# Optimization experiments

Measured on AMD Instinct MI355X. Metric: run time of the kernel, lower is better.

The kernel has to match this reference:

```python
import jax, jax.numpy as jnp
import numpy as np

B, C, H, W = 8, 512, 48, 48
DK = C // 8            # query/key dim
L = max(H, W)          # rel_pos_length == H == W
R = 2 * L - 1          # num relative shifts
N = H * W
EPS = 1e-5


def setup_inputs() -> dict:
    key = jax.random.key(0)
    ks = jax.random.split(key, 20)
    d = {
        "x": jax.random.normal(ks[0], (B, C, H, W), jnp.float32),
        "Wq": jax.random.normal(ks[1], (DK, C), jnp.float32) * 0.02,
        "bq": jnp.zeros((DK,), jnp.float32),
        "q_scale": jnp.ones((DK,), jnp.float32),
        "q_bias": jnp.zeros((DK,), jnp.float32),
        "Wk": jax.random.normal(ks[2], (DK, C), jnp.float32) * 0.02,
        "bk": jnp.zeros((DK,), jnp.float32),
        "k_scale": jnp.ones((DK,), jnp.float32),
        "k_bias": jnp.zeros((DK,), jnp.float32),
        "Wv": jax.random.normal(ks[3], (C, C), jnp.float32) * 0.02,
        "bv": jnp.zeros((C,), jnp.float32),
        "v_scale": jnp.ones((C,), jnp.float32),
        "v_bias": jnp.zeros((C,), jnp.float32),
        "rel_rows": jax.random.normal(ks[4], (R, DK), jnp.float32),
        "rel_columns": jax.random.normal(ks[5], (R, DK), jnp.float32),
        "bnr_scale": jnp.ones((C,), jnp.float32),
        "bnr_bias": jnp.zeros((C,), jnp.float32),
        "bnc_scale": jnp.ones((C,), jnp.float32),
        "bnc_bias": jnp.zeros((C,), jnp.float32),
        # gamma is a learned scalar (init 0 in torch; nonzero here so output != x)
        "gamma": jax.random.normal(ks[6], (1,), jnp.float32) * 0.1,
    }
    return d


def _bn(y, scale, bias):
    # train-mode BatchNorm2d: batch stats over (B,H,W), biased variance
    m = jnp.mean(y, axis=(0, 2, 3))
    v = jnp.mean((y - m[None, :, None, None]) ** 2, axis=(0, 2, 3))
    yn = (y - m[None, :, None, None]) * jax.lax.rsqrt(v + EPS)[None, :, None, None]
    return yn * scale[None, :, None, None] + bias[None, :, None, None]


def _conv_bn_relu(x, Wc, bc, scale, bias):
    y = jnp.einsum('bchw,oc->bohw', x, Wc) + bc[None, :, None, None]  # 1x1 conv
    return jax.nn.relu(_bn(y, scale, bias))


def _rel_P(l, rel_table):
    # compute_reindexing_tensor reduces to a one-hot over shift (i - x) since
    # |i-x| <= L always holds when L == l; Ih @ rel_table == gather by shift.
    x = jnp.arange(l)[:, None]
    i = jnp.arange(l)[None, :]
    idx = i - x + (L - 1)                 # (l, l) in [0, 2L-2]
    return rel_table[idx]                 # (l, l, DK)


def reference(x, Wq, bq, q_scale, q_bias, Wk, bk, k_scale, k_bias,
              Wv, bv, v_scale, v_bias, rel_rows, rel_columns,
              bnr_scale, bnr_bias, bnc_scale, bnc_bias, gamma):
    q = _conv_bn_relu(x, Wq, bq, q_scale, q_bias).reshape(B, DK, N)   # proj_query^T
    k = _conv_bn_relu(x, Wk, bk, k_scale, k_bias).reshape(B, DK, N)
    v = _conv_bn_relu(x, Wv, bv, v_scale, v_bias).reshape(B, C, N)

    energy = jnp.einsum('bdn,bdm->bnm', q, k)        # (B,N,N) = Q^T K (unscaled)
    attention = jax.nn.softmax(energy, axis=-1)
    out = jnp.einsum('bcj,bij->bci', v, attention)   # V A^T
    attn_mask = out.reshape(B, C, H, W)

    # relative position terms: Eh = V (Ph Q^T), Ew = V (Pw Q^T)
    Ph = _rel_P(H, rel_rows).reshape(N, DK)          # (N,DK) since H==W
    Mh = jnp.einsum('nd,bdm->bnm', Ph, q)
    Eh = jnp.einsum('bcn,bnm->bcm', v, Mh).reshape(B, C, H, W)
    Eh = _bn(Eh, bnr_scale, bnr_bias)

    Pw = _rel_P(W, rel_columns).reshape(N, DK)
    Mw = jnp.einsum('nd,bdm->bnm', Pw, q)
    Ew = jnp.einsum('bcn,bnm->bcm', v, Mw).reshape(B, C, H, W)
    Ew = _bn(Ew, bnc_scale, bnc_bias)

    attn_mask = attn_mask + Eh + Ew
    return gamma[0] * attn_mask + x
```

## Files before the change

### kernel.cpp

```cpp
#include <hip/hip_runtime.h>
#include <math.h>

#define BB   8
#define CIN  512
#define NSP  2304
#define OCH  640
#define LL   48

typedef __attribute__((ext_vector_type(8))) short bf16x8;
typedef __attribute__((ext_vector_type(8))) unsigned short u16x8;
typedef __attribute__((ext_vector_type(4))) float f32x4;

__device__ inline unsigned short f2bf(float f) {
  unsigned int u = __float_as_uint(f);
  unsigned int r = (u + 0x7fffu + ((u >> 16) & 1u)) >> 16;
  return (unsigned short)r;
}
__device__ inline float bf2f(unsigned short h) {
  return __uint_as_float(((unsigned int)h) << 16);
}


#define STAGE128x64(GP, LD, LDSN)                                              \
  {                                                                            \
    const unsigned short* gsrc_ = (GP);                                        \
    _Pragma("unroll") for (int cc_ = 0; cc_ < 4; cc_++) {                      \
      int base_ = w * 2048 + cc_ * 512;                                        \
      int row_ = w * 32 + cc_ * 8 + rsub;                                      \
      __builtin_amdgcn_global_load_lds(                                        \
          (const __attribute__((address_space(1))) void*)(gsrc_ +              \
              (size_t)row_ * (LD) + scolb),                                    \
          (__attribute__((address_space(3))) void*)&(LDSN)[base_], 16, 0, 0);  \
    }                                                                          \
  }

#define MFMA_STEP(APTR, BPTR)                                                  \
  _Pragma("unroll") for (int kk_ = 0; kk_ < 2; kk_++) {                        \
    bf16x8 af_[4], bf_[4];                                                     \
    int kcol_ = (((kk_ * 4 + (lane >> 4)) ^ (lane & 7)) * 8);                  \
    _Pragma("unroll") for (int m_ = 0; m_ < 4; m_++)                           \
      af_[m_] = *(const bf16x8*)&(APTR)[(wr * 64 + m_ * 16 + (lane & 15)) * 64 + kcol_]; \
    _Pragma("unroll") for (int n_ = 0; n_ < 4; n_++)                           \
      bf_[n_] = *(const bf16x8*)&(BPTR)[(wc * 64 + n_ * 16 + (lane & 15)) * 64 + kcol_]; \
    _Pragma("unroll") for (int m_ = 0; m_ < 4; m_++)                           \
      _Pragma("unroll") for (int n_ = 0; n_ < 4; n_++)                         \
        acc[m_][n_] = __builtin_amdgcn_mfma_f32_16x16x32_bf16(                 \
            af_[m_], bf_[n_], acc[m_][n_], 0, 0, 0);                           \
  }

#define MFMA_PROLOG()                                                          \
  const int tid = threadIdx.x;                                                 \
  const int lane = tid & 63;                                                   \
  const int w = tid >> 6;                                                      \
  const int wr = w >> 1, wc = w & 1;                                           \
  const int rsub = lane >> 3;                                                  \
  const int scolb = ((lane & 7) ^ rsub) * 8;                                   \
  f32x4 acc[4][4] = {};                                                        \
  (void)scolb; (void)rsub;

__global__ __launch_bounds__(256) void prep_all(
    const float* __restrict__ Wq, const float* __restrict__ bq,
    const float* __restrict__ Wk, const float* __restrict__ bk,
    const float* __restrict__ Wv, const float* __restrict__ bv,
    const float* __restrict__ rel_rows, const float* __restrict__ rel_cols,
    unsigned short* __restrict__ Wstb, float* __restrict__ bst,
    unsigned short* __restrict__ Pcatb) {
  int idx = blockIdx.x * 256 + threadIdx.x;
  if (idx < OCH * CIN) {
    int row = idx >> 9;
    float val;
    if (row < 64)       val = Wq[idx];
    else if (row < 128) val = Wk[idx - (64 << 9)];
    else                val = Wv[idx - (128 << 9)];
    Wstb[idx] = f2bf(val);
    if (idx < OCH) {
      float bval;
      if (idx < 64)       bval = bq[idx];
      else if (idx < 128) bval = bk[idx - 64];
      else                bval = bv[idx - 128];
      bst[idx] = bval;
    }
  } else {
    int p = idx - OCH * CIN;
    int dd = p / NSP;
    int n = p - dd * NSP;
    int xr = n / LL;
    int ic = n - xr * LL;
    int shift = ic - xr + (LL - 1);
    float val = (dd < 64) ? rel_rows[shift * 64 + dd]
                          : rel_cols[shift * 64 + (dd - 64)];
    Pcatb[p] = f2bf(val);
  }
}

__global__ __launch_bounds__(256) void transpose_x(
    const float* __restrict__ x, unsigned short* __restrict__ xTb) {
  __shared__ float t[64][65];
  const int n0 = blockIdx.x * 64;
  const int c0 = blockIdx.y * 64;
  const int b = blockIdx.z;
  const int j = threadIdx.x & 63;
  const int g = threadIdx.x >> 6;
  const float* xp = x + (size_t)b * CIN * NSP;
#pragma unroll
  for (int i = 0; i < 16; i++) {
    int cl = g * 16 + i;
    t[cl][j] = xp[(size_t)(c0 + cl) * NSP + n0 + j];
  }
  __syncthreads();
  unsigned short* op = xTb + (size_t)b * NSP * CIN;
#pragma unroll
  for (int i = 0; i < 16; i++) {
    int nl = g * 16 + i;
    op[(size_t)(n0 + nl) * CIN + c0 + j] = f2bf(t[j][nl]);
  }
}

__global__ __launch_bounds__(256) void proj_mfma(
    const unsigned short* __restrict__ Wstb, const float* __restrict__ bst,
    const unsigned short* __restrict__ xTb, unsigned short* __restrict__ y16,
    float* __restrict__ part1, float* __restrict__ part2) {
  __shared__ unsigned short As[8192];
  __shared__ unsigned short Bs[8192];
  int sw = ((blockIdx.x & 7) * 90) + (blockIdx.x >> 3);
  const int rb = sw % 5;
  const int nb = (sw / 5) % 18;
  const int b = sw / 90;
  const int r0 = rb * 128;
  const int n0 = nb * 128;
  MFMA_PROLOG();
  const unsigned short* A = Wstb + (size_t)r0 * CIN;
  const unsigned short* B = xTb + (size_t)b * NSP * CIN + (size_t)n0 * CIN;
  for (int k0 = 0; k0 < CIN; k0 += 64) {
    STAGE128x64(A + k0, CIN, As);
    STAGE128x64(B + k0, CIN, Bs);
    __syncthreads();
    MFMA_STEP(As, Bs);
    __syncthreads();
  }
  float* sp = (float*)As;
#pragma unroll
  for (int m = 0; m < 4; m++) {
#pragma unroll
    for (int r = 0; r < 4; r++) {
      int rl = wr * 64 + m * 16 + (lane >> 4) * 4 + r;
      int row = r0 + rl;
      float bias = bst[row];
      float s1 = 0.f, s2 = 0.f;
#pragma unroll
      for (int n = 0; n < 4; n++) {
        float yv = acc[m][n][r] + bias;
        s1 += yv;
        s2 += yv * yv;
        y16[((size_t)b * OCH + row) * NSP + n0 + wc * 64 + n * 16 + (lane & 15)] = f2bf(yv);
      }
#pragma unroll
      for (int off = 1; off < 16; off <<= 1) {
        s1 += __shfl_xor(s1, off);
        s2 += __shfl_xor(s2, off);
      }
      if ((lane & 15) == 0) {
        sp[rl * 2 + wc] = s1;
        sp[256 + rl * 2 + wc] = s2;
      }
    }
  }
  __syncthreads();
  if (tid < 128) {
    size_t pbase = ((size_t)b * 18 + nb) * OCH + r0 + tid;
    part1[pbase] = sp[tid * 2] + sp[tid * 2 + 1];
    part2[pbase] = sp[256 + tid * 2] + sp[256 + tid * 2 + 1];
  }
}

__global__ __launch_bounds__(256) void bn_finalize(
    const float* __restrict__ part1, const float* __restrict__ part2,
    const float* __restrict__ qs_, const float* __restrict__ qb_,
    const float* __restrict__ ks_, const float* __restrict__ kb_,
    const float* __restrict__ vs_, const float* __restrict__ vb_,
    float* __restrict__ chanA, float* __restrict__ chanB) {
  const int ch = blockIdx.x;
  const int tid = threadIdx.x;
  float s1 = 0.f, s2 = 0.f;
  for (int t = tid; t < 144; t += 256) {
    s1 += part1[(size_t)t * OCH + ch];
    s2 += part2[(size_t)t * OCH + ch];
  }
  __shared__ float sb[8];
#pragma unroll
  for (int off = 32; off > 0; off >>= 1) {
    s1 += __shfl_down(s1, off);
    s2 += __shfl_down(s2, off);
  }
  int lane = tid & 63, wid = tid >> 6;
  if (lane == 0) { sb[wid] = s1; sb[4 + wid] = s2; }
  __syncthreads();
  if (tid == 0) {
    float ts  = sb[0] + sb[1] + sb[2] + sb[3];
    float ts2 = sb[4] + sb[5] + sb[6] + sb[7];
    const float inv = 1.f / (float)(BB * NSP);
    float mean = ts * inv;
    float var  = ts2 * inv - mean * mean;
    float scale, bias;
    if (ch < 64)       { scale = qs_[ch];       bias = qb_[ch]; }
    else if (ch < 128) { scale = ks_[ch - 64];  bias = kb_[ch - 64]; }
    else               { scale = vs_[ch - 128]; bias = vb_[ch - 128]; }
    float a = scale * rsqrtf(var + 1e-5f);
    chanA[ch] = a;
    chanB[ch] = bias - mean * a;
  }
}

__global__ __launch_bounds__(256) void bnrelu_all(
    unsigned short* __restrict__ y16, const float* __restrict__ chanA,
    const float* __restrict__ chanB) {
  size_t i = ((size_t)blockIdx.x * 256 + threadIdx.x) * 8;
  int ch = (int)((i / NSP) % OCH);
  float a = chanA[ch], bo = chanB[ch];
  ushort4 u0 = *(ushort4*)&y16[i];
  ushort4 u1 = *(ushort4*)&y16[i + 4];
  ushort4 o0, o1;
  o0.x = f2bf(fmaxf(0.f, a * bf2f(u0.x) + bo));
  o0.y = f2bf(fmaxf(0.f, a * bf2f(u0.y) + bo));
  o0.z = f2bf(fmaxf(0.f, a * bf2f(u0.z) + bo));
  o0.w = f2bf(fmaxf(0.f, a * bf2f(u0.w) + bo));
  o1.x = f2bf(fmaxf(0.f, a * bf2f(u1.x) + bo));
  o1.y = f2bf(fmaxf(0.f, a * bf2f(u1.y) + bo));
  o1.z = f2bf(fmaxf(0.f, a * bf2f(u1.z) + bo));
  o1.w = f2bf(fmaxf(0.f, a * bf2f(u1.w) + bo));
  *(ushort4*)&y16[i] = o0;
  *(ushort4*)&y16[i + 4] = o1;
}

__global__ __launch_bounds__(256) void tr_qk(
    const unsigned short* __restrict__ y16, unsigned short* __restrict__ qTb,
    unsigned short* __restrict__ kTb) {
  __shared__ unsigned short t[64][72];
  const int n0 = blockIdx.x * 64;
  const int qk = blockIdx.y;
  const int b = blockIdx.z;
  const int j = threadIdx.x & 63;
  const int g = threadIdx.x >> 6;
#pragma unroll
  for (int i = 0; i < 16; i++) {
    int cl = g * 16 + i;
    t[cl][j] = y16[((size_t)b * OCH + qk * 64 + cl) * NSP + n0 + j];
  }
  __syncthreads();
  unsigned short* out = (qk == 0) ? qTb : kTb;
#pragma unroll
  for (int i = 0; i < 16; i++) {
    int nl = g * 16 + i;
    out[((size_t)b * NSP + n0 + nl) * 64 + j] = t[j][nl];
  }
}

__global__ __launch_bounds__(256) void qsum_kernel(
    const unsigned short* __restrict__ y16, float* __restrict__ qs) {
  int bd = blockIdx.x;
  int b = bd >> 6, d = bd & 63;
  const ushort4* p = (const ushort4*)(y16 + ((size_t)b * OCH + d) * NSP);
  float s = 0.f;
  for (int t = threadIdx.x; t < NSP / 4; t += 256) {
    ushort4 u = p[t];
    s += bf2f(u.x) + bf2f(u.y) + bf2f(u.z) + bf2f(u.w);
  }
  __shared__ float sb[4];
#pragma unroll
  for (int off = 32; off > 0; off >>= 1) s += __shfl_down(s, off);
  int lane = threadIdx.x & 63, wid = threadIdx.x >> 6;
  if (lane == 0) sb[wid] = s;
  __syncthreads();
  if (threadIdx.x == 0) qs[bd] = sb[0] + sb[1] + sb[2] + sb[3];
}

__global__ __launch_bounds__(256) void gq_mfma(
    const unsigned short* __restrict__ y16, float* __restrict__ Gqp) {
  __shared__ float wlds[4 * 4096];
  const int bx = blockIdx.x;
  const int b = bx >> 2, kc = bx & 3;
  const int tid = threadIdx.x;
  const int lane = tid & 63;
  const int w = tid >> 6;
  const unsigned short* q = y16 + (size_t)b * OCH * NSP;
  f32x4 acc[4][4] = {};
  for (int k0 = kc * 576 + w * 32; k0 < (kc + 1) * 576; k0 += 128) {
    bf16x8 fr[4];
#pragma unroll
    for (int f = 0; f < 4; f++) {
      int row = f * 16 + (lane & 15);
      fr[f] = *(const bf16x8*)&q[(size_t)row * NSP + k0 + (lane >> 4) * 8];
    }
#pragma unroll
    for (int fm = 0; fm < 4; fm++)
#pragma unroll
      for (int fn = 0; fn < 4; fn++)
        acc[fm][fn] = __builtin_amdgcn_mfma_f32_16x16x32_bf16(
            fr[fm], fr[fn], acc[fm][fn], 0, 0, 0);
  }
#pragma unroll
  for (int fm = 0; fm < 4; fm++)
#pragma unroll
    for (int fn = 0; fn < 4; fn++)
#pragma unroll
      for (int r = 0; r < 4; r++) {
        int d = fm * 16 + (lane >> 4) * 4 + r;
        int e = fn * 16 + (lane & 15);
        wlds[w * 4096 + d * 64 + e] = acc[fm][fn][r];
      }
  __syncthreads();
  for (int t = tid; t < 4096; t += 256)
    Gqp[(size_t)bx * 4096 + t] =
        wlds[t] + wlds[4096 + t] + wlds[8192 + t] + wlds[12288 + t];
}

__global__ __launch_bounds__(256) void energy_mfma(
    const unsigned short* __restrict__ qTb, const unsigned short* __restrict__ kTb,
    unsigned short* __restrict__ Pp, float* __restrict__ Ppart) {
  __shared__ unsigned short As[8192];
  __shared__ unsigned short Bs[8192];
  int sw = ((blockIdx.x & 7) * 324) + (blockIdx.x >> 3);
  const int jb = sw % 18;
  const int ib = (sw / 18) % 18;
  const int b = sw / 324;
  const int i0 = ib * 128;
  const int j0 = jb * 128;
  MFMA_PROLOG();
  STAGE128x64(qTb + ((size_t)b * NSP + i0) * 64, 64, As);
  STAGE128x64(kTb + ((size_t)b * NSP + j0) * 64, 64, Bs);
  __syncthreads();
  MFMA_STEP(As, Bs);
  __syncthreads();
  float* sp = (float*)As;
  unsigned short* pp = Pp + (size_t)b * NSP * NSP;
#pragma unroll
  for (int m = 0; m < 4; m++) {
#pragma unroll
    for (int r = 0; r < 4; r++) {
      int rl = wr * 64 + m * 16 + (lane >> 4) * 4 + r;
      int i = i0 + rl;
      float s1 = 0.f;
#pragma unroll
      for (int n = 0; n < 4; n++) {
        int j = j0 + wc * 64 + n * 16 + (lane & 15);
        unsigned short h = f2bf(__expf(acc[m][n][r]));
        pp[(size_t)i * NSP + j] = h;
        s1 += bf2f(h);
      }
#pragma unroll
      for (int off = 1; off < 16; off <<= 1) s1 += __shfl_xor(s1, off);
      if ((lane & 15) == 0) sp[rl * 2 + wc] = s1;
    }
  }
  __syncthreads();
  if (tid < 128)
    Ppart[((size_t)b * 18 + jb) * NSP + i0 + tid] = sp[tid * 2] + sp[tid * 2 + 1];
}

__global__ __launch_bounds__(256) void zred_kernel(
    const float* __restrict__ Ppart, float* __restrict__ rZ) {
  int row = blockIdx.x * 256 + threadIdx.x;
  int b = row / NSP, i = row % NSP;
  float s = 0.f;
#pragma unroll
  for (int jb = 0; jb < 18; jb++) s += Ppart[((size_t)b * 18 + jb) * NSP + i];
  rZ[row] = 1.f / s;
}

__global__ __launch_bounds__(256) void up_mfma(
    const unsigned short* __restrict__ y16, const unsigned short* __restrict__ Pcatb,
    float* __restrict__ Upart) {
  __shared__ unsigned short As[8192];
  __shared__ unsigned short Bs[8192];
  int sw = ((blockIdx.x & 7) * 24) + (blockIdx.x >> 3);
  const int cb = sw % 4;
  const int kc = (sw / 4) % 6;
  const int b = sw / 24;
  const int c0 = cb * 128;
  MFMA_PROLOG();
  const unsigned short* A = y16 + ((size_t)b * OCH + 128 + c0) * NSP;
  for (int k0 = kc * 384; k0 < kc * 384 + 384; k0 += 64) {
    STAGE128x64(A + k0, NSP, As);
    STAGE128x64(Pcatb + k0, NSP, Bs);
    __syncthreads();
    MFMA_STEP(As, Bs);
    __syncthreads();
  }
  float* up = Upart + ((size_t)kc * BB + b) * CIN * 128 + (size_t)c0 * 128;
#pragma unroll
  for (int m = 0; m < 4; m++)
#pragma unroll
    for (int r = 0; r < 4; r++) {
      int rl = wr * 64 + m * 16 + (lane >> 4) * 4 + r;
#pragma unroll
      for (int n = 0; n < 4; n++) {
        int col = wc * 64 + n * 16 + (lane & 15);
        up[(size_t)rl * 128 + col] = acc[m][n][r];
      }
    }
}

__global__ __launch_bounds__(256) void up_reduce(
    const float* __restrict__ Upart, float* __restrict__ Ucat) {
  size_t idx = (size_t)blockIdx.x * 256 + threadIdx.x;
  float s = 0.f;
#pragma unroll
  for (int kc = 0; kc < 6; kc++) s += Upart[(size_t)kc * 524288 + idx];
  Ucat[idx] = s;
}

__global__ __launch_bounds__(64) void rel_stats(
    const float* __restrict__ Ucat, const float* __restrict__ Gqp,
    const float* __restrict__ qs,
    const float* __restrict__ bnr_s, const float* __restrict__ bnr_b,
    const float* __restrict__ bnc_s, const float* __restrict__ bnc_b,
    float* __restrict__ gh, float* __restrict__ gw, float* __restrict__ offc) {
  const int c = blockIdx.x;
  const int d = threadIdx.x;
  __shared__ float su[2][64];
  float s1h = 0.f, s2h = 0.f, s1w = 0.f, s2w = 0.f;
  for (int b = 0; b < BB; b++) {
    size_t base = ((size_t)b * CIN + c) * 128;
    float uh = Ucat[base + d];
    float uw = Ucat[base + 64 + d];
    __syncthreads();
    su[0][d] = uh;
    su[1][d] = uw;
    __syncthreads();
    float th = 0.f, tw = 0.f;
#pragma unroll
    for (int kc = 0; kc < 4; kc++) {
      const float* G = Gqp + ((size_t)(b * 4 + kc)) * 4096 + d * 64;
      for (int e = 0; e < 64; e++) {
        float g = G[e];
        th += g * su[0][e];
        tw += g * su[1][e];
      }
    }
    float qsd = qs[b * 64 + d];
    s1h += uh * qsd;
    s2h += uh * th;
    s1w += uw * qsd;
    s2w += uw * tw;
  }
#pragma unroll
  for (int off = 32; off > 0; off >>= 1) {
    s1h += __shfl_down(s1h, off);
    s2h += __shfl_down(s2h, off);
    s1w += __shfl_down(s1w, off);
    s2w += __shfl_down(s2w, off);
  }
  if (d == 0) {
    const float inv = 1.f / (float)(BB * NSP);
    float mh = s1h * inv, vh = s2h * inv - mh * mh;
    float mw = s1w * inv, vw = s2w * inv - mw * mw;
    float gch = bnr_s[c] * rsqrtf(vh + 1e-5f);
    float gcw = bnc_s[c] * rsqrtf(vw + 1e-5f);
    gh[c] = gch;
    gw[c] = gcw;
    offc[c] = (bnr_b[c] - mh * gch) + (bnc_b[c] - mw * gcw);
  }
}

__global__ __launch_bounds__(256) void combine_u(
    const float* __restrict__ Ucat, const float* __restrict__ gh,
    const float* __restrict__ gw, unsigned short* __restrict__ Ucb) {
  int idx = blockIdx.x * 256 + threadIdx.x;
  int d = idx & 63;
  int c = (idx >> 6) & 511;
  int b = idx >> 15;
  size_t base = ((size_t)b * CIN + c) * 128;
  Ucb[idx] = f2bf(Ucat[base + d] * gh[c] + Ucat[base + 64 + d] * gw[c]);
}

__global__ __launch_bounds__(256) void attn_fused_gemm(
    const unsigned short* __restrict__ y16,
    const unsigned short* __restrict__ Pp,
    const float* __restrict__ rZ,
    const unsigned short* __restrict__ Ucb,
    const unsigned short* __restrict__ qTb,
    const float* __restrict__ offc,
    const float* __restrict__ gammap,
    const float* __restrict__ x,
    float* __restrict__ dst) {
  __shared__ unsigned short As[2][8192];
  __shared__ unsigned short Bs[2][8192];
  int sw = ((blockIdx.x & 7) * 72) + (blockIdx.x >> 3);
  const int cb = sw % 4;
  const int ib = (sw / 4) % 18;
  const int b = sw / 72;
  const int c0 = cb * 128;
  const int i0 = ib * 128;
  MFMA_PROLOG();
  const unsigned short* A = y16 + ((size_t)b * OCH + 128 + c0) * NSP;
  const unsigned short* B = Pp + (size_t)b * NSP * NSP + (size_t)i0 * NSP;
  const unsigned short* A2 = Ucb + (size_t)b * CIN * 64 + (size_t)c0 * 64;
  const unsigned short* B2 = qTb + (size_t)b * NSP * 64 + (size_t)i0 * 64;

  STAGE128x64(A, NSP, As[0]);
  STAGE128x64(B, NSP, Bs[0]);
  STAGE128x64(A + 64, NSP, As[1]);
  STAGE128x64(B + 64, NSP, Bs[1]);
  asm volatile("s_waitcnt vmcnt(8)" ::: "memory");
  __builtin_amdgcn_sched_barrier(0);
  __builtin_amdgcn_s_barrier();

  int cur = 0;
  for (int tt = 0; tt < 37; ++tt) {
    if (tt == 36) {
#pragma unroll
      for (int n = 0; n < 4; n++) {
        float rz = rZ[(size_t)b * NSP + i0 + wc * 64 + n * 16 + (lane & 15)];
#pragma unroll
        for (int m = 0; m < 4; m++)
#pragma unroll
          for (int r = 0; r < 4; r++) acc[m][n][r] *= rz;
      }
    }
    __builtin_amdgcn_s_setprio(1);
    MFMA_STEP(As[cur], Bs[cur]);
    __builtin_amdgcn_s_setprio(0);
    __builtin_amdgcn_sched_barrier(0);
    __builtin_amdgcn_s_barrier();
    if (tt + 2 < 36) {
      STAGE128x64(A + (tt + 2) * 64, NSP, As[cur]);
      STAGE128x64(B + (tt + 2) * 64, NSP, Bs[cur]);
      asm volatile("s_waitcnt vmcnt(8)" ::: "memory");
    } else if (tt + 2 == 36) {
      STAGE128x64(A2, 64, As[cur]);
      STAGE128x64(B2, 64, Bs[cur]);
      asm volatile("s_waitcnt vmcnt(8)" ::: "memory");
    } else {
      asm volatile("s_waitcnt vmcnt(0)" ::: "memory");
    }
    __builtin_amdgcn_sched_barrier(0);
    __builtin_amdgcn_s_barrier();
    cur ^= 1;
  }

  const float gmm = gammap[0];
  const float* xp = x + (size_t)b * CIN * NSP;
  float* dp = dst + (size_t)b * CIN * NSP;
#pragma unroll
  for (int m = 0; m < 4; m++) {
#pragma unroll
    for (int r = 0; r < 4; r++) {
      int c = c0 + wr * 64 + m * 16 + (lane >> 4) * 4 + r;
      float off = offc[c];
#pragma unroll
      for (int n = 0; n < 4; n++) {
        int i = i0 + wc * 64 + n * 16 + (lane & 15);
        size_t o = (size_t)c * NSP + i;
        dp[o] = gmm * (acc[m][n][r] + off) + xp[o];
      }
    }
  }
}

extern "C" void kernel_launch(void* const* d_in, const int* in_sizes, int n_in,
                              void* d_out, int out_size, void* d_ws, size_t ws_size,
                              hipStream_t stream) {
  const float* x        = (const float*)d_in[0];
  const float* Wq       = (const float*)d_in[1];
  const float* bq       = (const float*)d_in[2];
  const float* q_scale  = (const float*)d_in[3];
  const float* q_bias   = (const float*)d_in[4];
  const float* Wk       = (const float*)d_in[5];
  const float* bk       = (const float*)d_in[6];
  const float* k_scale  = (const float*)d_in[7];
  const float* k_bias   = (const float*)d_in[8];
  const float* Wv       = (const float*)d_in[9];
  const float* bv       = (const float*)d_in[10];
  const float* v_scale  = (const float*)d_in[11];
  const float* v_bias   = (const float*)d_in[12];
  const float* rel_rows = (const float*)d_in[13];
  const float* rel_cols = (const float*)d_in[14];
  const float* bnr_s    = (const float*)d_in[15];
  const float* bnr_b    = (const float*)d_in[16];
  const float* bnc_s    = (const float*)d_in[17];
  const float* bnc_b    = (const float*)d_in[18];
  const float* gamma    = (const float*)d_in[19];
  float* dst = (float*)d_out;

  float* ws = (float*)d_ws;
  size_t o = 0;
  unsigned short* Wstb = (unsigned short*)(ws + o); o += (size_t)OCH * CIN / 2;
  float* bst    = ws + o; o += 1024;
  float* chanA  = ws + o; o += 1024;
  float* chanB  = ws + o; o += 1024;
  unsigned short* Pcatb = (unsigned short*)(ws + o); o += (size_t)128 * NSP / 2;
  unsigned short* y16 = (unsigned short*)(ws + o); o += (size_t)BB * OCH * NSP / 2;
  unsigned short* xTb = (unsigned short*)(ws + o); o += (size_t)BB * NSP * CIN / 2;
  unsigned short* Pp  = (unsigned short*)(ws + o); o += (size_t)BB * NSP * NSP / 2;
  float* Ppart  = ws + o; o += (size_t)BB * 18 * NSP;
  float* rZ     = ws + o; o += (size_t)BB * NSP;
  float* Upart  = ws + o; o += (size_t)6 * BB * CIN * 128;
  float* Ucat   = ws + o; o += (size_t)BB * CIN * 128;
  float* Gqp    = ws + o; o += (size_t)32 * 4096;
  float* part1  = ws + o; o += (size_t)BB * 18 * OCH;
  float* part2  = ws + o; o += (size_t)BB * 18 * OCH;
  float* qs     = ws + o; o += 1024;
  float* gh     = ws + o; o += 1024;
  float* gw     = ws + o; o += 1024;
  float* offc   = ws + o; o += 1024;
  unsigned short* qTb = (unsigned short*)(ws + o); o += (size_t)BB * NSP * 64 / 2;
  unsigned short* kTb = (unsigned short*)(ws + o); o += (size_t)BB * NSP * 64 / 2;
  unsigned short* Ucb = (unsigned short*)(ws + o); o += (size_t)BB * CIN * 64 / 2;

  prep_all<<<(OCH * CIN + 128 * NSP) / 256, 256, 0, stream>>>(
      Wq, bq, Wk, bk, Wv, bv, rel_rows, rel_cols, Wstb, bst, Pcatb);
  transpose_x<<<dim3(NSP / 64, CIN / 64, BB), 256, 0, stream>>>(x, xTb);

  proj_mfma<<<720, 256, 0, stream>>>(Wstb, bst, xTb, y16, part1, part2);
  bn_finalize<<<OCH, 256, 0, stream>>>(part1, part2, q_scale, q_bias, k_scale,
                                       k_bias, v_scale, v_bias, chanA, chanB);
  bnrelu_all<<<(int)((size_t)BB * OCH * NSP / 8 / 256), 256, 0, stream>>>(y16, chanA, chanB);
  tr_qk<<<dim3(NSP / 64, 2, BB), 256, 0, stream>>>(y16, qTb, kTb);
  qsum_kernel<<<BB * 64, 256, 0, stream>>>(y16, qs);
  gq_mfma<<<32, 256, 0, stream>>>(y16, Gqp);

  energy_mfma<<<2592, 256, 0, stream>>>(qTb, kTb, Pp, Ppart);
  zred_kernel<<<BB * NSP / 256, 256, 0, stream>>>(Ppart, rZ);

  up_mfma<<<192, 256, 0, stream>>>(y16, Pcatb, Upart);
  up_reduce<<<2048, 256, 0, stream>>>(Upart, Ucat);
  rel_stats<<<CIN, 64, 0, stream>>>(Ucat, Gqp, qs, bnr_s, bnr_b, bnc_s, bnc_b,
                                    gh, gw, offc);
  combine_u<<<(BB * CIN * 64) / 256, 256, 0, stream>>>(Ucat, gh, gw, Ucb);

  attn_fused_gemm<<<576, 256, 0, stream>>>(y16, Pp, rZ, Ucb, qTb, offc, gamma, x, dst);
}
```

Measured before the change: 249.8 us.

## Double-buffer proj/up GEMMs, fuse rel-stats kernels, use 512-thread attention blocks

The projection and up GEMMs switch from a load-sync-compute loop with a single LDS buffer to a double-buffered prefetch pipeline with raised wave priority, so global loads overlap with MFMA work. The up_reduce, rel_stats and combine_u kernels are merged into one rel_finalize kernel, which removes two launches and the Ucat round trip through global memory. The final attention GEMM moves to 512 threads per block, with 8 waves each computing a 64x32 sub-tile and half the waves staging A while the other half stage B. The trade is more LDS per block and fewer accumulators per wave, which changes how many blocks fit per CU and how much latency each wave can hide.

```diff
diff --git a/kernel.cpp b/kernel.cpp
--- a/kernel.cpp
+++ b/kernel.cpp
@@ -31,6 +31,32 @@
           (const __attribute__((address_space(1))) void*)(gsrc_ +              \
               (size_t)row_ * (LD) + scolb),                                    \
           (__attribute__((address_space(3))) void*)&(LDSN)[base_], 16, 0, 0);  \
+    }                                                                          \
+  }
+
+#define STAGE8(GPA, LDA, LA, GPB, LDB, LB)                                     \
+  {                                                                            \
+    if (w < 4) {                                                               \
+      const unsigned short* gsrc_ = (GPA);                                     \
+      _Pragma("unroll") for (int cc_ = 0; cc_ < 4; cc_++) {                    \
+        int base_ = w * 2048 + cc_ * 512;                                      \
+        int row_ = w * 32 + cc_ * 8 + rsub;                                    \
+        __builtin_amdgcn_global_load_lds(                                      \
+            (const __attribute__((address_space(1))) void*)(gsrc_ +            \
+                (size_t)row_ * (LDA) + scolb),                                 \
+            (__attribute__((address_space(3))) void*)&(LA)[base_], 16, 0, 0);  \
+      }                                                                        \
+    } else {                                                                   \
+      const unsigned short* gsrc_ = (GPB);                                     \
+      int w2_ = w - 4;                                                         \
+      _Pragma("unroll") for (int cc_ = 0; cc_ < 4; cc_++) {                    \
+        int base_ = w2_ * 2048 + cc_ * 512;                                    \
+        int row_ = w2_ * 32 + cc_ * 8 + rsub;                                  \
+        __builtin_amdgcn_global_load_lds(                                      \
+            (const __attribute__((address_space(1))) void*)(gsrc_ +            \
+                (size_t)row_ * (LDB) + scolb),                                 \
+            (__attribute__((address_space(3))) void*)&(LB)[base_], 16, 0, 0);  \
+      }                                                                        \
     }                                                                          \
   }
 
@@ -48,6 +74,20 @@
             af_[m_], bf_[n_], acc[m_][n_], 0, 0, 0);                           \
   }
 
+#define MFMA_STEP8(APTR, BPTR)                                                 \
+  _Pragma("unroll") for (int kk_ = 0; kk_ < 2; kk_++) {                        \
+    bf16x8 af_[4], bf_[2];                                                     \
+    int kcol_ = (((kk_ * 4 + (lane >> 4)) ^ (lane & 7)) * 8);                  \
+    _Pragma("unroll") for (int m_ = 0; m_ < 4; m_++)                           \
+      af_[m_] = *(const bf16x8*)&(APTR)[(wr * 64 + m_ * 16 + (lane & 15)) * 64 + kcol_]; \
+    _Pragma("unroll") for (int n_ = 0; n_ < 2; n_++)                           \
+      bf_[n_] = *(const bf16x8*)&(BPTR)[(wc * 32 + n_ * 16 + (lane & 15)) * 64 + kcol_]; \
+    _Pragma("unroll") for (int m_ = 0; m_ < 4; m_++)                           \
+      _Pragma("unroll") for (int n_ = 0; n_ < 2; n_++)                         \
+        acc[m_][n_] = __builtin_amdgcn_mfma_f32_16x16x32_bf16(                 \
+            af_[m_], bf_[n_], acc[m_][n_], 0, 0, 0);                           \
+  }
+
 #define MFMA_PROLOG()                                                          \
   const int tid = threadIdx.x;                                                 \
   const int lane = tid & 63;                                                   \
@@ -56,7 +96,7 @@
   const int rsub = lane >> 3;                                                  \
   const int scolb = ((lane & 7) ^ rsub) * 8;                                   \
   f32x4 acc[4][4] = {};                                                        \
-  (void)scolb; (void)rsub;
+  (void)scolb; (void)rsub; (void)wr; (void)wc;
 
 __global__ __launch_bounds__(256) void prep_all(
     const float* __restrict__ Wq, const float* __restrict__ bq,
@@ -120,8 +160,8 @@
     const unsigned short* __restrict__ Wstb, const float* __restrict__ bst,
     const unsigned short* __restrict__ xTb, unsigned short* __restrict__ y16,
     float* __restrict__ part1, float* __restrict__ part2) {
-  __shared__ unsigned short As[8192];
-  __shared__ unsigned short Bs[8192];
+  __shared__ unsigned short As[2][8192];
+  __shared__ unsigned short Bs[2][8192];
   int sw = ((blockIdx.x & 7) * 90) + (blockIdx.x >> 3);
   const int rb = sw % 5;
   const int nb = (sw / 5) % 18;
@@ -131,14 +171,35 @@
   MFMA_PROLOG();
   const unsigned short* A = Wstb + (size_t)r0 * CIN;
   const unsigned short* B = xTb + (size_t)b * NSP * CIN + (size_t)n0 * CIN;
-  for (int k0 = 0; k0 < CIN; k0 += 64) {
-    STAGE128x64(A + k0, CIN, As);
-    STAGE128x64(B + k0, CIN, Bs);
-    __syncthreads();
-    MFMA_STEP(As, Bs);
-    __syncthreads();
-  }
-  float* sp = (float*)As;
+
+  STAGE128x64(A, CIN, As[0]);
+  STAGE128x64(B, CIN, Bs[0]);
+  STAGE128x64(A + 64, CIN, As[1]);
+  STAGE128x64(B + 64, CIN, Bs[1]);
+  asm volatile("s_waitcnt vmcnt(8)" ::: "memory");
+  __builtin_amdgcn_sched_barrier(0);
+  __builtin_amdgcn_s_barrier();
+
+  int cur = 0;
+  for (int t = 0; t < 8; ++t) {
+    __builtin_amdgcn_s_setprio(1);
+    MFMA_STEP(As[cur], Bs[cur]);
+    __builtin_amdgcn_s_setprio(0);
+    __builtin_amdgcn_sched_barrier(0);
+    __builtin_amdgcn_s_barrier();
+    if (t + 2 < 8) {
+      STAGE128x64(A + (t + 2) * 64, CIN, As[cur]);
+      STAGE128x64(B + (t + 2) * 64, CIN, Bs[cur]);
+      asm volatile("s_waitcnt vmcnt(8)" ::: "memory");
+    } else {
+      asm volatile("s_waitcnt vmcnt(0)" ::: "memory");
+    }
+    __builtin_amdgcn_sched_barrier(0);
+    __builtin_amdgcn_s_barrier();
+    cur ^= 1;
+  }
+
+  float* sp = (float*)&As[0][0];
 #pragma unroll
   for (int m = 0; m < 4; m++) {
 #pragma unroll
@@ -370,22 +431,44 @@
 __global__ __launch_bounds__(256) void up_mfma(
     const unsigned short* __restrict__ y16, const unsigned short* __restrict__ Pcatb,
     float* __restrict__ Upart) {
-  __shared__ unsigned short As[8192];
-  __shared__ unsigned short Bs[8192];
+  __shared__ unsigned short As[2][8192];
+  __shared__ unsigned short Bs[2][8192];
   int sw = ((blockIdx.x & 7) * 24) + (blockIdx.x >> 3);
   const int cb = sw % 4;
   const int kc = (sw / 4) % 6;
   const int b = sw / 24;
   const int c0 = cb * 128;
   MFMA_PROLOG();
-  const unsigned short* A = y16 + ((size_t)b * OCH + 128 + c0) * NSP;
-  for (int k0 = kc * 384; k0 < kc * 384 + 384; k0 += 64) {
-    STAGE128x64(A + k0, NSP, As);
-    STAGE128x64(Pcatb + k0, NSP, Bs);
-    __syncthreads();
-    MFMA_STEP(As, Bs);
-    __syncthreads();
-  }
+  const unsigned short* A = y16 + ((size_t)b * OCH + 128 + c0) * NSP + kc * 384;
+  const unsigned short* B = Pcatb + kc * 384;
+
+  STAGE128x64(A, NSP, As[0]);
+  STAGE128x64(B, NSP, Bs[0]);
+  STAGE128x64(A + 64, NSP, As[1]);
+  STAGE128x64(B + 64, NSP, Bs[1]);
+  asm volatile("s_waitcnt vmcnt(8)" ::: "memory");
+  __builtin_amdgcn_sched_barrier(0);
+  __builtin_amdgcn_s_barrier();
+
+  int cur = 0;
+  for (int t = 0; t < 6; ++t) {
+    __builtin_amdgcn_s_setprio(1);
+    MFMA_STEP(As[cur], Bs[cur]);
+    __builtin_amdgcn_s_setprio(0);
+    __builtin_amdgcn_sched_barrier(0);
+    __builtin_amdgcn_s_barrier();
+    if (t + 2 < 6) {
+      STAGE128x64(A + (t + 2) * 64, NSP, As[cur]);
+      STAGE128x64(B + (t + 2) * 64, NSP, Bs[cur]);
+      asm volatile("s_waitcnt vmcnt(8)" ::: "memory");
+    } else {
+      asm volatile("s_waitcnt vmcnt(0)" ::: "memory");
+    }
+    __builtin_amdgcn_sched_barrier(0);
+    __builtin_amdgcn_s_barrier();
+    cur ^= 1;
+  }
+
   float* up = Upart + ((size_t)kc * BB + b) * CIN * 128 + (size_t)c0 * 128;
 #pragma unroll
   for (int m = 0; m < 4; m++)
@@ -400,80 +483,73 @@
     }
 }
 
-__global__ __launch_bounds__(256) void up_reduce(
-    const float* __restrict__ Upart, float* __restrict__ Ucat) {
-  size_t idx = (size_t)blockIdx.x * 256 + threadIdx.x;
-  float s = 0.f;
-#pragma unroll
-  for (int kc = 0; kc < 6; kc++) s += Upart[(size_t)kc * 524288 + idx];
-  Ucat[idx] = s;
-}
-
-__global__ __launch_bounds__(64) void rel_stats(
-    const float* __restrict__ Ucat, const float* __restrict__ Gqp,
+__global__ __launch_bounds__(256) void rel_finalize(
+    const float* __restrict__ Upart, const float* __restrict__ Gqp,
     const float* __restrict__ qs,
     const float* __restrict__ bnr_s, const float* __restrict__ bnr_b,
     const float* __restrict__ bnc_s, const float* __restrict__ bnc_b,
-    float* __restrict__ gh, float* __restrict__ gw, float* __restrict__ offc) {
+    float* __restrict__ offc, unsigned short* __restrict__ Ucb) {
   const int c = blockIdx.x;
-  const int d = threadIdx.x;
-  __shared__ float su[2][64];
-  float s1h = 0.f, s2h = 0.f, s1w = 0.f, s2w = 0.f;
-  for (int b = 0; b < BB; b++) {
-    size_t base = ((size_t)b * CIN + c) * 128;
-    float uh = Ucat[base + d];
-    float uw = Ucat[base + 64 + d];
-    __syncthreads();
-    su[0][d] = uh;
-    su[1][d] = uw;
-    __syncthreads();
-    float th = 0.f, tw = 0.f;
-#pragma unroll
-    for (int kc = 0; kc < 4; kc++) {
-      const float* G = Gqp + ((size_t)(b * 4 + kc)) * 4096 + d * 64;
-      for (int e = 0; e < 64; e++) {
-        float g = G[e];
-        th += g * su[0][e];
-        tw += g * su[1][e];
-      }
-    }
-    float qsd = qs[b * 64 + d];
-    s1h += uh * qsd;
-    s2h += uh * th;
-    s1w += uw * qsd;
-    s2w += uw * tw;
-  }
-#pragma unroll
-  for (int off = 32; off > 0; off >>= 1) {
-    s1h += __shfl_down(s1h, off);
-    s2h += __shfl_down(s2h, off);
-    s1w += __shfl_down(s1w, off);
-    s2w += __shfl_down(s2w, off);
-  }
-  if (d == 0) {
-    const float inv = 1.f / (float)(BB * NSP);
-    float mh = s1h * inv, vh = s2h * inv - mh * mh;
-    float mw = s1w * inv, vw = s2w * inv - mw * mw;
-    float gch = bnr_s[c] * rsqrtf(vh + 1e-5f);
-    float gcw = bnc_s[c] * rsqrtf(vw + 1e-5f);
-    gh[c] = gch;
-    gw[c] = gcw;
-    offc[c] = (bnr_b[c] - mh * gch) + (bnc_b[c] - mw * gcw);
-  }
-}
-
-__global__ __launch_bounds__(256) void combine_u(
-    const float* __restrict__ Ucat, const float* __restrict__ gh,
-    const float* __restrict__ gw, unsigned short* __restrict__ Ucb) {
-  int idx = blockIdx.x * 256 + threadIdx.x;
-  int d = idx & 63;
-  int c = (idx >> 6) & 511;
-  int b = idx >> 15;
-  size_t base = ((size_t)b * CIN + c) * 128;
-  Ucb[idx] = f2bf(Ucat[base + d] * gh[c] + Ucat[base + 64 + d] * gw[c]);
-}
-
-__global__ __launch_bounds__(256) void attn_fused_gemm(
+  const int tid = threadIdx.x;
+  __shared__ float U[8][128];
+  __shared__ float ghw[2];
+  for (int t = tid; t < 1024; t += 256) {
+    int b = t >> 7, dd = t & 127;
+    float s = 0.f;
+#pragma unroll
+    for (int kc = 0; kc < 6; kc++)
+      s += Upart[(((size_t)kc * BB + b) * CIN + c) * 128 + dd];
+    U[b][dd] = s;
+  }
+  __syncthreads();
+  if (tid < 64) {
+    const int d = tid;
+    float s1h = 0.f, s2h = 0.f, s1w = 0.f, s2w = 0.f;
+    for (int b = 0; b < BB; b++) {
+      float uh = U[b][d], uw = U[b][64 + d];
+      float th = 0.f, tw = 0.f;
+#pragma unroll
+      for (int kc = 0; kc < 4; kc++) {
+        const float* G = Gqp + ((size_t)(b * 4 + kc)) * 4096 + d * 64;
+        for (int e = 0; e < 64; e++) {
+          float g = G[e];
+          th += g * U[b][e];
+          tw += g * U[b][64 + e];
+        }
+      }
+      float qsd = qs[b * 64 + d];
+      s1h += uh * qsd;
+      s2h += uh * th;
+      s1w += uw * qsd;
+      s2w += uw * tw;
+    }
+#pragma unroll
+    for (int off = 32; off > 0; off >>= 1) {
+      s1h += __shfl_down(s1h, off);
+      s2h += __shfl_down(s2h, off);
+      s1w += __shfl_down(s1w, off);
+      s2w += __shfl_down(s2w, off);
+    }
+    if (d == 0) {
+      const float inv = 1.f / (float)(BB * NSP);
+      float mh = s1h * inv, vh = s2h * inv - mh * mh;
+      float mw = s1w * inv, vw = s2w * inv - mw * mw;
+      float gch = bnr_s[c] * rsqrtf(vh + 1e-5f);
+      float gcw = bnc_s[c] * rsqrtf(vw + 1e-5f);
+      ghw[0] = gch;
+      ghw[1] = gcw;
+      offc[c] = (bnr_b[c] - mh * gch) + (bnc_b[c] - mw * gcw);
+    }
+  }
+  __syncthreads();
+  for (int t = tid; t < 512; t += 256) {
+    int b = t >> 6, d = t & 63;
+    Ucb[((size_t)b * CIN + c) * 64 + d] =
+        f2bf(U[b][d] * ghw[0] + U[b][64 + d] * ghw[1]);
+  }
+}
+
+__global__ __launch_bounds__(512) void attn_fused_gemm(
     const unsigned short* __restrict__ y16,
     const unsigned short* __restrict__ Pp,
     const float* __restrict__ rZ,
@@ -491,17 +567,22 @@
   const int b = sw / 72;
   const int c0 = cb * 128;
   const int i0 = ib * 128;
-  MFMA_PROLOG();
+  const int tid = threadIdx.x;
+  const int lane = tid & 63;
+  const int w = tid >> 6;
+  const int wr = w >> 2, wc = w & 3;
+  const int rsub = lane >> 3;
+  const int scolb = ((lane & 7) ^ rsub) * 8;
+  f32x4 acc[4][2] = {};
+
   const unsigned short* A = y16 + ((size_t)b * OCH + 128 + c0) * NSP;
   const unsigned short* B = Pp + (size_t)b * NSP * NSP + (size_t)i0 * NSP;
   const unsigned short* A2 = Ucb + (size_t)b * CIN * 64 + (size_t)c0 * 64;
   const unsigned short* B2 = qTb + (size_t)b * NSP * 64 + (size_t)i0 * 64;
 
-  STAGE128x64(A, NSP, As[0]);
-  STAGE128x64(B, NSP, Bs[0]);
-  STAGE128x64(A + 64, NSP, As[1]);
-  STAGE128x64(B + 64, NSP, Bs[1]);
-  asm volatile("s_waitcnt vmcnt(8)" ::: "memory");
+  STAGE8(A, NSP, As[0], B, NSP, Bs[0]);
+  STAGE8(A + 64, NSP, As[1], B + 64, NSP, Bs[1]);
+  asm volatile("s_waitcnt vmcnt(4)" ::: "memory");
   __builtin_amdgcn_sched_barrier(0);
   __builtin_amdgcn_s_barrier();
 
@@ -509,8 +590,8 @@
   for (int tt = 0; tt < 37; ++tt) {
     if (tt == 36) {
 #pragma unroll
-      for (int n = 0; n < 4; n++) {
-        float rz = rZ[(size_t)b * NSP + i0 + wc * 64 + n * 16 + (lane & 15)];
+      for (int n = 0; n < 2; n++) {
+        float rz = rZ[(size_t)b * NSP + i0 + wc * 32 + n * 16 + (lane & 15)];
 #pragma unroll
         for (int m = 0; m < 4; m++)
 #pragma unroll
@@ -518,18 +599,16 @@
       }
     }
     __builtin_amdgcn_s_setprio(1);
-    MFMA_STEP(As[cur], Bs[cur]);
+    MFMA_STEP8(As[cur], Bs[cur]);
     __builtin_amdgcn_s_setprio(0);
     __builtin_amdgcn_sched_barrier(0);
     __builtin_amdgcn_s_barrier();
     if (tt + 2 < 36) {
-      STAGE128x64(A + (tt + 2) * 64, NSP, As[cur]);
-      STAGE128x64(B + (tt + 2) * 64, NSP, Bs[cur]);
-      asm volatile("s_waitcnt vmcnt(8)" ::: "memory");
+      STAGE8(A + (tt + 2) * 64, NSP, As[cur], B + (tt + 2) * 64, NSP, Bs[cur]);
+      asm volatile("s_waitcnt vmcnt(4)" ::: "memory");
     } else if (tt + 2 == 36) {
-      STAGE128x64(A2, 64, As[cur]);
-      STAGE128x64(B2, 64, Bs[cur]);
-      asm volatile("s_waitcnt vmcnt(8)" ::: "memory");
+      STAGE8(A2, 64, As[cur], B2, 64, Bs[cur]);
+      asm volatile("s_waitcnt vmcnt(4)" ::: "memory");
     } else {
       asm volatile("s_waitcnt vmcnt(0)" ::: "memory");
     }
@@ -548,8 +627,8 @@
       int c = c0 + wr * 64 + m * 16 + (lane >> 4) * 4 + r;
       float off = offc[c];
 #pragma unroll
-      for (int n = 0; n < 4; n++) {
-        int i = i0 + wc * 64 + n * 16 + (lane & 15);
+      for (int n = 0; n < 2; n++) {
+        int i = i0 + wc * 32 + n * 16 + (lane & 15);
         size_t o = (size_t)c * NSP + i;
         dp[o] = gmm * (acc[m][n][r] + off) + xp[o];
       }
@@ -595,13 +674,10 @@
   float* Ppart  = ws + o; o += (size_t)BB * 18 * NSP;
   float* rZ     = ws + o; o += (size_t)BB * NSP;
   float* Upart  = ws + o; o += (size_t)6 * BB * CIN * 128;
-  float* Ucat   = ws + o; o += (size_t)BB * CIN * 128;
   float* Gqp    = ws + o; o += (size_t)32 * 4096;
   float* part1  = ws + o; o += (size_t)BB * 18 * OCH;
   float* part2  = ws + o; o += (size_t)BB * 18 * OCH;
   float* qs     = ws + o; o += 1024;
-  float* gh     = ws + o; o += 1024;
-  float* gw     = ws + o; o += 1024;
   float* offc   = ws + o; o += 1024;
   unsigned short* qTb = (unsigned short*)(ws + o); o += (size_t)BB * NSP * 64 / 2;
   unsigned short* kTb = (unsigned short*)(ws + o); o += (size_t)BB * NSP * 64 / 2;
@@ -623,10 +699,8 @@
   zred_kernel<<<BB * NSP / 256, 256, 0, stream>>>(Ppart, rZ);
 
   up_mfma<<<192, 256, 0, stream>>>(y16, Pcatb, Upart);
-  up_reduce<<<2048, 256, 0, stream>>>(Upart, Ucat);
-  rel_stats<<<CIN, 64, 0, stream>>>(Ucat, Gqp, qs, bnr_s, bnr_b, bnc_s, bnc_b,
-                                    gh, gw, offc);
-  combine_u<<<(BB * CIN * 64) / 256, 256, 0, stream>>>(Ucat, gh, gw, Ucb);
-
-  attn_fused_gemm<<<576, 256, 0, stream>>>(y16, Pp, rZ, Ucb, qTb, offc, gamma, x, dst);
-}
+  rel_finalize<<<CIN, 256, 0, stream>>>(Upart, Gqp, qs, bnr_s, bnr_b,
+                                        bnc_s, bnc_b, offc, Ucb);
+
+  attn_fused_gemm<<<576, 512, 0, stream>>>(y16, Pp, rZ, Ucb, qTb, offc, gamma, x, dst);
+}
```

Result: faster. 237.9 us (-4.8%).
